# Performance work log

Hardware: AMD Instinct MI355X
Metric: run time of the kernel (lower is better)

Reference implementation:

```python
import jax, jax.numpy as jnp
import numpy as np


def setup_inputs() -> dict:
    key = jax.random.key(0)
    ks = jax.random.split(key, 9)
    B, Q, K, F, C = 16, 2048, 2048, 128, 2
    q = jax.random.normal(ks[0], (B, Q, F), dtype=jnp.float32)
    k = jax.random.normal(ks[1], (B, K, F), dtype=jnp.float32)
    v = jax.random.normal(ks[2], (B, K, F), dtype=jnp.float32)
    coords_q = jax.random.uniform(ks[3], (B, Q, C), dtype=jnp.float32)
    coords_k = jax.random.uniform(ks[4], (B, K, C), dtype=jnp.float32)
    attn_mask = jax.random.randint(ks[5], (B, Q, K), 0, 2).astype(jnp.bool_)
    alibi_mask = jax.random.randint(ks[6], (B, Q, K), 0, 2).astype(jnp.bool_)
    bias_scale = jax.random.uniform(ks[7], (1,), dtype=jnp.float32)  # nn.Parameter(torch.rand(1))
    running_mean = jnp.ones((1,), dtype=jnp.float32)  # RunningMeanScaler buffer (eval mode)
    return {"q": q, "k": k, "v": v, "coords_q": coords_q, "coords_k": coords_k,
            "attn_mask": attn_mask, "alibi_mask": alibi_mask,
            "bias_scale": bias_scale, "running_mean": running_mean}


def reference(q, k, v, coords_q, coords_k, attn_mask, alibi_mask, bias_scale, running_mean):
    # [b,q,k] attention logits
    scale = jnp.asarray(k.shape[-1], q.dtype) ** -0.5
    weight_logits = jnp.einsum('bqf,bkf->bqk', q, k) * scale
    # pairwise coordinate distances [b,q,k]
    diff = coords_q[:, :, None, :] - coords_k[:, None, :, :]
    distances = jnp.sqrt(jnp.sum(diff * diff, axis=-1))
    scaled_distances = (distances / running_mean) * bias_scale  # broadcast scalars
    masked_distances = jnp.where(alibi_mask, jnp.zeros((), distances.dtype), scaled_distances)
    weights = jax.nn.softmax(weight_logits, axis=-1)
    masked = jnp.where(attn_mask, jnp.zeros((), weights.dtype), weights - masked_distances)
    attention = jnp.einsum('bqk,bkf->bqf', masked, v)
    return attention
```

## Files before the change

kernel.cpp:

```cpp
#include <hip/hip_runtime.h>
#include <stdint.h>

#define B_  16
#define QL  2048
#define KL  2048
#define FD  128
#define BQ  64
#define BK  32
#define NSTEP (KL/BK)

#define KSTR  136
#define VTOFF 4352
#define VTSTR 36
#define BUFS  8960
#define PSTR  40
#define WS_HALF (B_*KL*FD)

typedef __attribute__((ext_vector_type(8))) short bf16x8;
typedef __attribute__((ext_vector_type(4))) float f32x4;

__device__ __forceinline__ unsigned short f2b(float f) {
  union { float f; unsigned u; } x; x.f = f;
  return (unsigned short)((x.u + 0x8000u) >> 16);
}

__global__ __launch_bounds__(256) void conv_k(const float* __restrict__ kp,
                                              unsigned short* __restrict__ kb) {
  int idx = (blockIdx.x * 256 + threadIdx.x) * 4;
  float4 u = *(const float4*)(kp + idx);
  ushort4 s4; s4.x = f2b(u.x); s4.y = f2b(u.y); s4.z = f2b(u.z); s4.w = f2b(u.w);
  *(ushort4*)(kb + idx) = s4;
}

__global__ __launch_bounds__(256) void conv_vt(const float* __restrict__ vp,
                                               unsigned short* __restrict__ vt) {
  __shared__ float tl[32 * 132];
  const int t = threadIdx.x, b = blockIdx.x >> 6, kt = blockIdx.x & 63;
  const int r = t >> 3, f0 = (t & 7) * 16;
  const float* src = vp + ((long long)(b * KL + kt * 32 + r)) * FD + f0;
  #pragma unroll
  for (int i = 0; i < 4; ++i)
    *(float4*)&tl[r * 132 + f0 + 4 * i] = *(const float4*)(src + 4 * i);
  __syncthreads();
  const int f = t >> 1, half = t & 1;
  bf16x8 o0, o1;
  #pragma unroll
  for (int j = 0; j < 8; ++j)  o0[j] = (short)f2b(tl[(half * 16 + j) * 132 + f]);
  #pragma unroll
  for (int j = 0; j < 8; ++j)  o1[j] = (short)f2b(tl[(half * 16 + 8 + j) * 132 + f]);
  unsigned short* dst = vt + ((long long)((b * 64 + kt) * FD + f)) * 32 + half * 16;
  *(bf16x8*)dst = o0;
  *(bf16x8*)(dst + 8) = o1;
}

__global__ __launch_bounds__(256, 2) void alibi_attn(
    const unsigned short* __restrict__ kbp,
    const unsigned short* __restrict__ vtp,
    const float* __restrict__ qp,
    const float* __restrict__ cqp,
    const float* __restrict__ ckp,
    const int* __restrict__ amp,
    const int* __restrict__ almp,
    const float* __restrict__ bsp,
    const float* __restrict__ rmp,
    float* __restrict__ outp)
{
  __shared__ unsigned short kv[2 * BUFS];
  __shared__ unsigned short plds[4][2][16 * PSTR];

  const int t    = threadIdx.x;
  const int w    = t >> 6;
  const int lane = t & 63;
  const int l15  = lane & 15;
  const int q4   = lane >> 4;

  const int bid  = blockIdx.x;
  const int xcd  = bid & 7, slot = bid >> 3;
  const int b    = (xcd << 1) | (slot >> 5);
  const int qbase = (slot & 31) * BQ;

  const float bscale = bsp[0] / rmp[0];
  const float sl2 = 0.08838834764831845f * 1.44269504089f;

  const int kr_st = t >> 3, kc_st = (t & 7) * 16;
  const int vf_st = t >> 1, vh_st = (t & 1) * 16;

  {
    const float* qg = qp + ((long long)(b * QL + qbase)) * FD;
    #pragma unroll
    for (int i = 0; i < 8; ++i) {
      int idx = t + 256 * i;
      float4 u = ((const float4*)qg)[idx];
      int row = idx >> 5, col = (idx & 31) * 4;
      ushort4 s4; s4.x = f2b(u.x); s4.y = f2b(u.y); s4.z = f2b(u.z); s4.w = f2b(u.w);
      *(ushort4*)&kv[row * KSTR + col] = s4;
    }
  }
  __syncthreads();
  bf16x8 qfrag[4];
  {
    const int m = w * 16 + l15;
    #pragma unroll
    for (int fs = 0; fs < 4; ++fs)
      qfrag[fs] = *(const bf16x8*)&kv[m * KSTR + fs * 32 + q4 * 8];
  }
  float cqx[4], cqy[4];
  long long mrow_base[4];
  #pragma unroll
  for (int r = 0; r < 4; ++r) {
    const int qg_ = qbase + w * 16 + q4 * 4 + r;
    float2 c2 = *(const float2*)(cqp + ((long long)(b * QL + qg_)) * 2);
    cqx[r] = c2.x; cqy[r] = c2.y;
    mrow_base[r] = ((long long)(b * QL + qg_)) * KL;
  }
  __syncthreads();

  const unsigned short* kgb = kbp + (long long)b * KL * FD;
  const unsigned short* vgb = vtp + (long long)b * KL * FD;

  int   amv[2][8], alv[2][8];
  float ckxv[2][2], ckyv[2][2];
  bf16x8 kreg[2][2], vreg[2][2];
  #pragma unroll
  for (int s = 0; s < 2; ++s) {
    const int kg = s * 16 + l15;
    #pragma unroll
    for (int r = 0; r < 4; ++r) {
      amv[0][s * 4 + r] = __builtin_nontemporal_load(amp + mrow_base[r] + kg);
      alv[0][s * 4 + r] = __builtin_nontemporal_load(almp + mrow_base[r] + kg);
    }
    float2 c2 = *(const float2*)(ckp + ((long long)(b * KL + kg)) * 2);
    ckxv[0][s] = c2.x; ckyv[0][s] = c2.y;
  }
  {
    bf16x8 k0l = *(const bf16x8*)(kgb + kr_st * FD + kc_st);
    bf16x8 k1l = *(const bf16x8*)(kgb + kr_st * FD + kc_st + 8);
    bf16x8 v0l = *(const bf16x8*)(vgb + t * 16);
    bf16x8 v1l = *(const bf16x8*)(vgb + t * 16 + 8);
    *(bf16x8*)&kv[kr_st * KSTR + kc_st]     = k0l;
    *(bf16x8*)&kv[kr_st * KSTR + kc_st + 8] = k1l;
    *(bf16x8*)&kv[VTOFF + vf_st * VTSTR + vh_st]     = v0l;
    *(bf16x8*)&kv[VTOFF + vf_st * VTSTR + vh_st + 8] = v1l;
    kreg[1][0] = *(const bf16x8*)(kgb + (BK + kr_st) * FD + kc_st);
    kreg[1][1] = *(const bf16x8*)(kgb + (BK + kr_st) * FD + kc_st + 8);
    vreg[1][0] = *(const bf16x8*)(vgb + BK * FD + t * 16);
    vreg[1][1] = *(const bf16x8*)(vgb + BK * FD + t * 16 + 8);
  }
  __syncthreads();

  f32x4 O1[8], O2[8];
  #pragma unroll
  for (int n = 0; n < 8; ++n) {
    O1[n] = (f32x4){0.f, 0.f, 0.f, 0.f};
    O2[n] = (f32x4){0.f, 0.f, 0.f, 0.f};
  }
  float lsum[4] = {0.f, 0.f, 0.f, 0.f};

  #pragma unroll 2
  for (int kt = 0; kt < NSTEP; ++kt) {
    const int cur = kt & 1, nxt = cur ^ 1;
    const unsigned short* kb = kv + cur * BUFS;
    unsigned short*       nb = kv + nxt * BUFS;

    const int ktf = (kt + 2 < NSTEP) ? (kt + 2) : (NSTEP - 1);
    kreg[cur][0] = *(const bf16x8*)(kgb + (ktf * BK + kr_st) * FD + kc_st);
    kreg[cur][1] = *(const bf16x8*)(kgb + (ktf * BK + kr_st) * FD + kc_st + 8);
    vreg[cur][0] = *(const bf16x8*)(vgb + ktf * (BK * FD) + t * 16);
    vreg[cur][1] = *(const bf16x8*)(vgb + ktf * (BK * FD) + t * 16 + 8);

    const int ktm = (kt + 1 < NSTEP) ? (kt + 1) : kt;
    #pragma unroll
    for (int s = 0; s < 2; ++s) {
      const int kg = ktm * BK + s * 16 + l15;
      #pragma unroll
      for (int r = 0; r < 4; ++r) {
        amv[nxt][s * 4 + r] = __builtin_nontemporal_load(amp + mrow_base[r] + kg);
        alv[nxt][s * 4 + r] = __builtin_nontemporal_load(almp + mrow_base[r] + kg);
      }
      float2 c2 = *(const float2*)(ckp + ((long long)(b * KL + kg)) * 2);
      ckxv[nxt][s] = c2.x; ckyv[nxt][s] = c2.y;
    }

    f32x4 S0 = (f32x4){0.f, 0.f, 0.f, 0.f};
    f32x4 S1 = (f32x4){0.f, 0.f, 0.f, 0.f};
    #pragma unroll
    for (int fs = 0; fs < 4; ++fs) {
      bf16x8 kb0 = *(const bf16x8*)&kb[(l15)      * KSTR + fs * 32 + q4 * 8];
      bf16x8 kb1 = *(const bf16x8*)&kb[(16 + l15) * KSTR + fs * 32 + q4 * 8];
      S0 = __builtin_amdgcn_mfma_f32_16x16x32_bf16(qfrag[fs], kb0, S0, 0, 0, 0);
      S1 = __builtin_amdgcn_mfma_f32_16x16x32_bf16(qfrag[fs], kb1, S1, 0, 0, 0);
    }

    #pragma unroll
    for (int s = 0; s < 2; ++s) {
      const f32x4 Sv = s ? S1 : S0;
      #pragma unroll
      for (int r = 0; r < 4; ++r) {
        int am = amv[cur][s * 4 + r], al = alv[cur][s * 4 + r];
        float e = __builtin_amdgcn_exp2f(Sv[r] * sl2);
        lsum[r] += e;
        float dx = cqx[r] - ckxv[cur][s], dy = cqy[r] - ckyv[cur][s];
        float d  = sqrtf(fmaf(dx, dx, dy * dy)) * bscale;
        float wv = am ? 0.f : e;
        float tv = (am | al) ? 0.f : d;
        const int mm = q4 * 4 + r, c = s * 16 + l15;
        plds[w][0][mm * PSTR + c] = f2b(wv);
        plds[w][1][mm * PSTR + c] = f2b(tv);
      }
    }

    bf16x8 aw = *(const bf16x8*)&plds[w][0][l15 * PSTR + q4 * 8];
    bf16x8 at = *(const bf16x8*)&plds[w][1][l15 * PSTR + q4 * 8];
    #pragma unroll
    for (int n = 0; n < 8; ++n) {
      bf16x8 vb = *(const bf16x8*)&kb[VTOFF + (n * 16 + l15) * VTSTR + q4 * 8];
      O1[n] = __builtin_amdgcn_mfma_f32_16x16x32_bf16(aw, vb, O1[n], 0, 0, 0);
      O2[n] = __builtin_amdgcn_mfma_f32_16x16x32_bf16(at, vb, O2[n], 0, 0, 0);
    }

    *(bf16x8*)&nb[kr_st * KSTR + kc_st]     = kreg[nxt][0];
    *(bf16x8*)&nb[kr_st * KSTR + kc_st + 8] = kreg[nxt][1];
    *(bf16x8*)&nb[VTOFF + vf_st * VTSTR + vh_st]     = vreg[nxt][0];
    *(bf16x8*)&nb[VTOFF + vf_st * VTSTR + vh_st + 8] = vreg[nxt][1];

    asm volatile("s_waitcnt lgkmcnt(0)\n\ts_barrier" ::: "memory");
  }

  #pragma unroll
  for (int off = 1; off < 16; off <<= 1) {
    #pragma unroll
    for (int r = 0; r < 4; ++r) lsum[r] += __shfl_xor(lsum[r], off, 64);
  }
  float linv[4];
  #pragma unroll
  for (int r = 0; r < 4; ++r) linv[r] = 1.0f / lsum[r];

  #pragma unroll
  for (int n = 0; n < 8; ++n) {
    #pragma unroll
    for (int r = 0; r < 4; ++r) {
      const int qg_ = qbase + w * 16 + q4 * 4 + r;
      const int f   = n * 16 + l15;
      float val = O1[n][r] * linv[r] - O2[n][r];
      __builtin_nontemporal_store(val, outp + ((long long)(b * QL + qg_)) * FD + f);
    }
  }
}

extern "C" void kernel_launch(void* const* d_in, const int* in_sizes, int n_in,
                              void* d_out, int out_size, void* d_ws, size_t ws_size,
                              hipStream_t stream) {
  const float* q   = (const float*)d_in[0];
  const float* k   = (const float*)d_in[1];
  const float* v   = (const float*)d_in[2];
  const float* cq  = (const float*)d_in[3];
  const float* ck  = (const float*)d_in[4];
  const int*   am  = (const int*)d_in[5];
  const int*   alm = (const int*)d_in[6];
  const float* bs  = (const float*)d_in[7];
  const float* rm  = (const float*)d_in[8];
  float*       out = (float*)d_out;

  unsigned short* kb = (unsigned short*)d_ws;
  unsigned short* vt = kb + WS_HALF;

  hipLaunchKernelGGL(conv_k,  dim3(WS_HALF / 1024), dim3(256), 0, stream, k, kb);
  hipLaunchKernelGGL(conv_vt, dim3(B_ * 64),        dim3(256), 0, stream, v, vt);

  dim3 grid(B_ * (QL / BQ));
  dim3 block(256);
  hipLaunchKernelGGL(alibi_attn, grid, block, 0, stream,
                     kb, vt, q, cq, ck, am, alm, bs, rm, out);
}
```

Before: 657.0 us.

## Transpose QK MFMA so P stays in registers, vectorize mask loads

Swaps the MFMA operand order so each lane holds one query row across four consecutive keys. This lets the attn/alibi mask and key-coordinate loads become 16-byte vector loads instead of scalar gathers. The P and T tiles are packed with v_cvt_pk_bf16 and rearranged into the PV A-operand layout with cross-lane shuffles, removing the per-wave LDS staging buffer and its writes and reads. The row-sum reduction changes to match the new layout. In exchange it adds about 16 bpermute-style shuffles and selects per tile, and its correctness depends on the MFMA output layout mapping being exactly right.

```diff
diff --git a/kernel.cpp b/kernel.cpp
--- a/kernel.cpp
+++ b/kernel.cpp
@@ -13,15 +13,22 @@
 #define VTOFF 4352
 #define VTSTR 36
 #define BUFS  8960
-#define PSTR  40
 #define WS_HALF (B_*KL*FD)
 
 typedef __attribute__((ext_vector_type(8))) short bf16x8;
 typedef __attribute__((ext_vector_type(4))) float f32x4;
+typedef __attribute__((ext_vector_type(4))) int   i32x4;
+typedef __attribute__((ext_vector_type(4))) unsigned int u32x4;
 
 __device__ __forceinline__ unsigned short f2b(float f) {
   union { float f; unsigned u; } x; x.f = f;
   return (unsigned short)((x.u + 0x8000u) >> 16);
+}
+
+__device__ __forceinline__ unsigned cvt_pk_bf16(float lo, float hi) {
+  unsigned r;
+  asm("v_cvt_pk_bf16_f32 %0, %1, %2" : "=v"(r) : "v"(lo), "v"(hi));
+  return r;
 }
 
 __global__ __launch_bounds__(256) void conv_k(const float* __restrict__ kp,
@@ -66,7 +73,6 @@
     float* __restrict__ outp)
 {
   __shared__ unsigned short kv[2 * BUFS];
-  __shared__ unsigned short plds[4][2][16 * PSTR];
 
   const int t    = threadIdx.x;
   const int w    = t >> 6;
@@ -104,33 +110,29 @@
     for (int fs = 0; fs < 4; ++fs)
       qfrag[fs] = *(const bf16x8*)&kv[m * KSTR + fs * 32 + q4 * 8];
   }
-  float cqx[4], cqy[4];
-  long long mrow_base[4];
-  #pragma unroll
-  for (int r = 0; r < 4; ++r) {
-    const int qg_ = qbase + w * 16 + q4 * 4 + r;
-    float2 c2 = *(const float2*)(cqp + ((long long)(b * QL + qg_)) * 2);
-    cqx[r] = c2.x; cqy[r] = c2.y;
-    mrow_base[r] = ((long long)(b * QL + qg_)) * KL;
-  }
+  const int qrow = qbase + w * 16 + l15;
+  float cqx, cqy;
+  {
+    float2 c2 = *(const float2*)(cqp + ((long long)(b * QL + qrow)) * 2);
+    cqx = c2.x; cqy = c2.y;
+  }
+  const long long mrow = (long long)(b * QL + qrow) * KL;
   __syncthreads();
 
   const unsigned short* kgb = kbp + (long long)b * KL * FD;
   const unsigned short* vgb = vtp + (long long)b * KL * FD;
 
-  int   amv[2][8], alv[2][8];
-  float ckxv[2][2], ckyv[2][2];
+  i32x4 amv[2][2], alv[2][2];
+  f32x4 ckf[2][2][2];
   bf16x8 kreg[2][2], vreg[2][2];
+  const int klane0 = 4 * q4;
   #pragma unroll
   for (int s = 0; s < 2; ++s) {
-    const int kg = s * 16 + l15;
-    #pragma unroll
-    for (int r = 0; r < 4; ++r) {
-      amv[0][s * 4 + r] = __builtin_nontemporal_load(amp + mrow_base[r] + kg);
-      alv[0][s * 4 + r] = __builtin_nontemporal_load(almp + mrow_base[r] + kg);
-    }
-    float2 c2 = *(const float2*)(ckp + ((long long)(b * KL + kg)) * 2);
-    ckxv[0][s] = c2.x; ckyv[0][s] = c2.y;
+    const int k0 = s * 16 + klane0;
+    amv[0][s] = __builtin_nontemporal_load((const i32x4*)(amp + mrow + k0));
+    alv[0][s] = __builtin_nontemporal_load((const i32x4*)(almp + mrow + k0));
+    ckf[0][s][0] = *(const f32x4*)(ckp + ((long long)(b * KL + k0)) * 2);
+    ckf[0][s][1] = *(const f32x4*)(ckp + ((long long)(b * KL + k0)) * 2 + 4);
   }
   {
     bf16x8 k0l = *(const bf16x8*)(kgb + kr_st * FD + kc_st);
@@ -154,7 +156,11 @@
     O1[n] = (f32x4){0.f, 0.f, 0.f, 0.f};
     O2[n] = (f32x4){0.f, 0.f, 0.f, 0.f};
   }
-  float lsum[4] = {0.f, 0.f, 0.f, 0.f};
+  float lsum = 0.f;
+
+  const int srcA = l15 + ((q4 & 1) << 5);
+  const int srcB = srcA + 16;
+  const bool lowhalf = (q4 < 2);
 
   #pragma unroll 2
   for (int kt = 0; kt < NSTEP; ++kt) {
@@ -171,14 +177,11 @@
     const int ktm = (kt + 1 < NSTEP) ? (kt + 1) : kt;
     #pragma unroll
     for (int s = 0; s < 2; ++s) {
-      const int kg = ktm * BK + s * 16 + l15;
-      #pragma unroll
-      for (int r = 0; r < 4; ++r) {
-        amv[nxt][s * 4 + r] = __builtin_nontemporal_load(amp + mrow_base[r] + kg);
-        alv[nxt][s * 4 + r] = __builtin_nontemporal_load(almp + mrow_base[r] + kg);
-      }
-      float2 c2 = *(const float2*)(ckp + ((long long)(b * KL + kg)) * 2);
-      ckxv[nxt][s] = c2.x; ckyv[nxt][s] = c2.y;
+      const int kg = ktm * BK + s * 16 + klane0;
+      amv[nxt][s] = __builtin_nontemporal_load((const i32x4*)(amp + mrow + kg));
+      alv[nxt][s] = __builtin_nontemporal_load((const i32x4*)(almp + mrow + kg));
+      ckf[nxt][s][0] = *(const f32x4*)(ckp + ((long long)(b * KL + kg)) * 2);
+      ckf[nxt][s][1] = *(const f32x4*)(ckp + ((long long)(b * KL + kg)) * 2 + 4);
     }
 
     f32x4 S0 = (f32x4){0.f, 0.f, 0.f, 0.f};
@@ -187,30 +190,60 @@
     for (int fs = 0; fs < 4; ++fs) {
       bf16x8 kb0 = *(const bf16x8*)&kb[(l15)      * KSTR + fs * 32 + q4 * 8];
       bf16x8 kb1 = *(const bf16x8*)&kb[(16 + l15) * KSTR + fs * 32 + q4 * 8];
-      S0 = __builtin_amdgcn_mfma_f32_16x16x32_bf16(qfrag[fs], kb0, S0, 0, 0, 0);
-      S1 = __builtin_amdgcn_mfma_f32_16x16x32_bf16(qfrag[fs], kb1, S1, 0, 0, 0);
-    }
-
+      S0 = __builtin_amdgcn_mfma_f32_16x16x32_bf16(kb0, qfrag[fs], S0, 0, 0, 0);
+      S1 = __builtin_amdgcn_mfma_f32_16x16x32_bf16(kb1, qfrag[fs], S1, 0, 0, 0);
+    }
+
+    float wvv[2][4], tvv[2][4];
     #pragma unroll
     for (int s = 0; s < 2; ++s) {
       const f32x4 Sv = s ? S1 : S0;
       #pragma unroll
       for (int r = 0; r < 4; ++r) {
-        int am = amv[cur][s * 4 + r], al = alv[cur][s * 4 + r];
         float e = __builtin_amdgcn_exp2f(Sv[r] * sl2);
-        lsum[r] += e;
-        float dx = cqx[r] - ckxv[cur][s], dy = cqy[r] - ckyv[cur][s];
+        lsum += e;
+        const float ckx = ckf[cur][s][r >> 1][(r & 1) * 2];
+        const float cky = ckf[cur][s][r >> 1][(r & 1) * 2 + 1];
+        float dx = cqx - ckx, dy = cqy - cky;
         float d  = sqrtf(fmaf(dx, dx, dy * dy)) * bscale;
-        float wv = am ? 0.f : e;
-        float tv = (am | al) ? 0.f : d;
-        const int mm = q4 * 4 + r, c = s * 16 + l15;
-        plds[w][0][mm * PSTR + c] = f2b(wv);
-        plds[w][1][mm * PSTR + c] = f2b(tv);
+        int am = amv[cur][s][r], al = alv[cur][s][r];
+        wvv[s][r] = am ? 0.f : e;
+        tvv[s][r] = (am | al) ? 0.f : d;
       }
     }
 
-    bf16x8 aw = *(const bf16x8*)&plds[w][0][l15 * PSTR + q4 * 8];
-    bf16x8 at = *(const bf16x8*)&plds[w][1][l15 * PSTR + q4 * 8];
+    unsigned aX0 = cvt_pk_bf16(wvv[0][0], wvv[0][1]);
+    unsigned aX1 = cvt_pk_bf16(wvv[0][2], wvv[0][3]);
+    unsigned aX2 = cvt_pk_bf16(wvv[1][0], wvv[1][1]);
+    unsigned aX3 = cvt_pk_bf16(wvv[1][2], wvv[1][3]);
+    unsigned tX0 = cvt_pk_bf16(tvv[0][0], tvv[0][1]);
+    unsigned tX1 = cvt_pk_bf16(tvv[0][2], tvv[0][3]);
+    unsigned tX2 = cvt_pk_bf16(tvv[1][0], tvv[1][1]);
+    unsigned tX3 = cvt_pk_bf16(tvv[1][2], tvv[1][3]);
+
+    u32x4 wa, ta;
+    {
+      int y0, y2;
+      y0 = __shfl((int)aX0, srcA); y2 = __shfl((int)aX2, srcA);
+      wa[0] = (unsigned)(lowhalf ? y0 : y2);
+      y0 = __shfl((int)aX1, srcA); y2 = __shfl((int)aX3, srcA);
+      wa[1] = (unsigned)(lowhalf ? y0 : y2);
+      y0 = __shfl((int)aX0, srcB); y2 = __shfl((int)aX2, srcB);
+      wa[2] = (unsigned)(lowhalf ? y0 : y2);
+      y0 = __shfl((int)aX1, srcB); y2 = __shfl((int)aX3, srcB);
+      wa[3] = (unsigned)(lowhalf ? y0 : y2);
+      y0 = __shfl((int)tX0, srcA); y2 = __shfl((int)tX2, srcA);
+      ta[0] = (unsigned)(lowhalf ? y0 : y2);
+      y0 = __shfl((int)tX1, srcA); y2 = __shfl((int)tX3, srcA);
+      ta[1] = (unsigned)(lowhalf ? y0 : y2);
+      y0 = __shfl((int)tX0, srcB); y2 = __shfl((int)tX2, srcB);
+      ta[2] = (unsigned)(lowhalf ? y0 : y2);
+      y0 = __shfl((int)tX1, srcB); y2 = __shfl((int)tX3, srcB);
+      ta[3] = (unsigned)(lowhalf ? y0 : y2);
+    }
+    bf16x8 aw = __builtin_bit_cast(bf16x8, wa);
+    bf16x8 at = __builtin_bit_cast(bf16x8, ta);
+
     #pragma unroll
     for (int n = 0; n < 8; ++n) {
       bf16x8 vb = *(const bf16x8*)&kb[VTOFF + (n * 16 + l15) * VTSTR + q4 * 8];
@@ -226,14 +259,11 @@
     asm volatile("s_waitcnt lgkmcnt(0)\n\ts_barrier" ::: "memory");
   }
 
-  #pragma unroll
-  for (int off = 1; off < 16; off <<= 1) {
-    #pragma unroll
-    for (int r = 0; r < 4; ++r) lsum[r] += __shfl_xor(lsum[r], off, 64);
-  }
+  lsum += __shfl_xor(lsum, 16, 64);
+  lsum += __shfl_xor(lsum, 32, 64);
   float linv[4];
   #pragma unroll
-  for (int r = 0; r < 4; ++r) linv[r] = 1.0f / lsum[r];
+  for (int r = 0; r < 4; ++r) linv[r] = 1.0f / __shfl(lsum, q4 * 4 + r, 64);
 
   #pragma unroll
   for (int n = 0; n < 8; ++n) {
```

Measured after the change: 676.0 us. 2.9% more time.
